# Optimization experiments

Measured on AMD Instinct MI355X. Metric: run time of the kernel, lower is better.

The kernel has to match this reference:

```python
import jax, jax.numpy as jnp
import numpy as np

B, H, N = 128, 512, 1024

def setup_inputs() -> dict:
    key = jax.random.key(0)
    ks = jax.random.split(key, 9)
    s = 1.0 / np.sqrt(H)
    return {
        "mc_hidden": jax.random.normal(ks[0], (B, H), jnp.float32),
        "sn_hidden": jax.random.normal(ks[1], (B, H, N), jnp.float32),
        "attn_W": jax.random.normal(ks[2], (H, 2 * H), jnp.float32) * s,
        "attn_v": jax.random.normal(ks[3], (H,), jnp.float32) * s,
        "ptr_v": jax.random.normal(ks[4], (H,), jnp.float32) * s,
        "fc1_W": jax.random.normal(ks[5], (H, 2 * H), jnp.float32) * s,
        "fc1_b": jax.random.normal(ks[6], (H,), jnp.float32) * s,
        "fc2_W": jax.random.normal(ks[7], (H, H), jnp.float32) * s,
        "fc2_b": jax.random.normal(ks[8], (H,), jnp.float32) * s,
    }


def reference(mc_hidden, sn_hidden, attn_W, attn_v, ptr_v, fc1_W, fc1_b, fc2_W, fc2_b):
    # ---- Attention (Bahdanau-style additive scoring) ----
    # hidden: (B, 2H, N) = cat(sn_hidden, mc expanded along N) on dim 1
    mc_exp = jnp.broadcast_to(mc_hidden[:, :, None], sn_hidden.shape)  # (B,H,N)
    hidden = jnp.concatenate((sn_hidden, mc_exp), axis=1)              # (B,2H,N)
    # W @ hidden -> (B,H,N); v @ tanh(.) -> (B,N)
    scores = jnp.einsum('h,bhn->bn', attn_v,
                        jnp.tanh(jnp.einsum('hk,bkn->bhn', attn_W, hidden)))
    attns = jax.nn.softmax(scores, axis=-1)                            # (B,N)
    # ---- Context + pointer scoring ----
    context = jnp.einsum('bn,bhn->bh', attns, sn_hidden)               # (B,H)
    x = jnp.concatenate((mc_hidden, context), axis=1)                  # (B,2H)
    out = jax.nn.relu(x @ fc1_W.T + fc1_b)                             # (B,H)
    out = jax.nn.relu(out @ fc2_W.T + fc2_b)                           # (B,H)
    probs = jnp.einsum('h,bhn->bn', ptr_v,
                       jnp.tanh(sn_hidden + out[:, :, None]))          # (B,N)
    return probs
```

## Files before the change

### kernel.cpp

```cpp
#include <hip/hip_runtime.h>
#include <hip/hip_bf16.h>

#define Bn 128
#define Hd 512
#define Nn 1024

typedef __attribute__((ext_vector_type(8))) short short8;
typedef __attribute__((ext_vector_type(4))) float f32x4;

#define GLOAD_LDS16(gptr, lptr)                                                     \
    __builtin_amdgcn_global_load_lds(                                               \
        (const __attribute__((address_space(1))) void*)(gptr),                      \
        (__attribute__((address_space(3))) void*)(lptr), 16, 0, 0)

__device__ __forceinline__ unsigned pack_bf2(float a, float b) {
    __hip_bfloat162 h = __float22bfloat162_rn(float2{a, b});
    unsigned u;
    __builtin_memcpy(&u, &h, 4);
    return u;
}

__device__ __forceinline__ float wave_sum(float v) {
    v += __shfl_xor(v, 32);
    v += __shfl_xor(v, 16);
    v += __shfl_xor(v, 8);
    v += __shfl_xor(v, 4);
    v += __shfl_xor(v, 2);
    v += __shfl_xor(v, 1);
    return v;
}

__device__ __forceinline__ float tanh_fast(float x) {
    float e = __expf(2.0f * x);
    return 1.0f - 2.0f * __builtin_amdgcn_rcpf(e + 1.0f);
}

__global__ void pre_kernel(const float* __restrict__ attn_W,
                           const float* __restrict__ mc,
                           unsigned short* __restrict__ Wb,
                           float* __restrict__ mc_term) {
    if (blockIdx.x < 128) {
        int idx = (blockIdx.x * 256 + threadIdx.x) * 8;
        int h = idx >> 9;
        int k = idx & 511;
        const float* p = attn_W + (size_t)h * 1024 + k;
        float4 v0 = *(const float4*)p;
        float4 v1 = *(const float4*)(p + 4);
        unsigned u[4] = {pack_bf2(v0.x, v0.y), pack_bf2(v0.z, v0.w),
                         pack_bf2(v1.x, v1.y), pack_bf2(v1.z, v1.w)};
        *(uint4*)(Wb + idx) = *(uint4*)u;
        return;
    }
    int wg = ((blockIdx.x - 128) * 256 + threadIdx.x) >> 6;
    int lane = threadIdx.x & 63;
    int b = wg >> 9;
    int h = wg & 511;
    const float* m = mc + b * Hd + lane * 8;
    const float* w = attn_W + (size_t)h * 1024 + 512 + lane * 8;
    float4 m0 = *(const float4*)m, m1 = *(const float4*)(m + 4);
    float4 w0 = *(const float4*)w, w1 = *(const float4*)(w + 4);
    float acc = m0.x * w0.x + m0.y * w0.y + m0.z * w0.z + m0.w * w0.w +
                m1.x * w1.x + m1.y * w1.y + m1.z * w1.z + m1.w * w1.w;
    acc = wave_sum(acc);
    if (lane == 0) mc_term[b * Hd + h] = acc;
}

__global__ __launch_bounds__(512, 4)
void attn_score_kernel(const float* __restrict__ sn,
                       const unsigned short* __restrict__ Wb,
                       const float* __restrict__ attn_v,
                       const float* __restrict__ mc_term,
                       float* __restrict__ scores_part) {
    __shared__ __align__(16) unsigned short A_lds[256 * 64];
    __shared__ __align__(16) unsigned short B_lds[128 * 64];
    __shared__ float av_s[256];
    __shared__ float mct_s[256];
    __shared__ float ssum[128];

    const int bid = blockIdx.x;
    const int b = bid >> 4;
    const int mh = (bid >> 3) & 1;
    const int n0 = (bid & 7) << 7;
    const int tid = threadIdx.x;
    const int lane = tid & 63;
    const int wid = tid >> 6;
    const int wr = wid >> 1;
    const int wc = wid & 1;
    const int quad = lane >> 4;
    const int l15 = lane & 15;

    if (tid < 256) {
        av_s[tid] = attn_v[mh * 256 + tid];
        mct_s[tid] = mc_term[b * Hd + mh * 256 + tid];
    }
    if (tid < 128) ssum[tid] = 0.f;

    f32x4 acc[4][4];
#pragma unroll
    for (int i = 0; i < 4; ++i)
#pragma unroll
        for (int j = 0; j < 4; ++j) {
            f32x4 z = {0.f, 0.f, 0.f, 0.f};
            acc[i][j] = z;
        }

    const int r8 = lane >> 3;
    const int csw = ((lane & 7) ^ r8) * 16;
    const char* Wg = (const char*)Wb + (size_t)(mh * 256) * 1024;
    const int key = l15 & 7;

    const int bswz = ((wid ^ (lane & 7)) * 16);
    const float* snB = sn + (size_t)b * Hd * Nn + (size_t)(8 * wid) * Nn + n0 + lane;

    for (int k0 = 0; k0 < 512; k0 += 64) {
#pragma unroll
        for (int i = 0; i < 4; ++i) {
            const int row = wid * 32 + i * 8;
            GLOAD_LDS16(Wg + (size_t)(row + r8) * 1024 + k0 * 2 + csw,
                        (char*)A_lds + row * 128);
        }
        {
            const float* pk = snB + (size_t)k0 * Nn;
#pragma unroll
            for (int j = 0; j < 2; ++j) {
                const int n = lane + 64 * j;
                const float* p = pk + 64 * j;
                float v0 = p[0 * Nn], v1 = p[1 * Nn], v2 = p[2 * Nn], v3 = p[3 * Nn];
                float v4 = p[4 * Nn], v5 = p[5 * Nn], v6 = p[6 * Nn], v7 = p[7 * Nn];
                unsigned kp[4] = {pack_bf2(v0, v1), pack_bf2(v2, v3),
                                  pack_bf2(v4, v5), pack_bf2(v6, v7)};
                *(uint4*)((char*)B_lds + n * 128 + bswz) = *(uint4*)kp;
            }
        }
        __syncthreads();
        __builtin_amdgcn_s_setprio(1);
#pragma unroll
        for (int kk = 0; kk < 2; ++kk) {
            const int cb = quad + kk * 4;
            short8 bfr[4], afr[4];
#pragma unroll
            for (int nt = 0; nt < 4; ++nt) {
                const int nl = wc * 64 + nt * 16 + l15;
                bfr[nt] = *(const short8*)((const char*)B_lds + nl * 128 + ((cb ^ key) * 16));
            }
#pragma unroll
            for (int mt = 0; mt < 4; ++mt) {
                const int m = wr * 64 + mt * 16 + l15;
                afr[mt] = *(const short8*)((const char*)A_lds + m * 128 + ((cb ^ key) * 16));
            }
#pragma unroll
            for (int mt = 0; mt < 4; ++mt)
#pragma unroll
                for (int nt = 0; nt < 4; ++nt)
                    acc[mt][nt] = __builtin_amdgcn_mfma_f32_16x16x32_bf16(afr[mt], bfr[nt], acc[mt][nt], 0, 0, 0);
        }
        __builtin_amdgcn_s_setprio(0);
        __syncthreads();
    }

    float s[4] = {0.f, 0.f, 0.f, 0.f};
#pragma unroll
    for (int mt = 0; mt < 4; ++mt) {
        int hb = wr * 64 + mt * 16 + quad * 4;
#pragma unroll
        for (int r = 0; r < 4; ++r) {
            float av = av_s[hb + r];
            float mcv = mct_s[hb + r];
#pragma unroll
            for (int nt = 0; nt < 4; ++nt)
                s[nt] += av * tanh_fast(acc[mt][nt][r] + mcv);
        }
    }
#pragma unroll
    for (int nt = 0; nt < 4; ++nt) {
        float v = s[nt];
        v += __shfl_xor(v, 16);
        v += __shfl_xor(v, 32);
        if (lane < 16) atomicAdd(&ssum[wc * 64 + nt * 16 + l15], v);
    }
    __syncthreads();
    if (tid < 128)
        scores_part[((size_t)mh * Bn + b) * Nn + n0 + tid] = ssum[tid];
}

__global__ void softmax_context_kernel(const float* __restrict__ sn,
                                       const float* __restrict__ scores_part,
                                       float* __restrict__ context) {
    int b = blockIdx.x >> 3;
    int h0 = (blockIdx.x & 7) << 6;
    int t = threadIdx.x;
    int lane = t & 63, wid = t >> 6;
    __shared__ float red[4];
    __shared__ float a_s[1024];

    const float* s0 = scores_part + (size_t)b * Nn;
    const float* s1 = scores_part + ((size_t)Bn + b) * Nn;
    float v[4];
#pragma unroll
    for (int i = 0; i < 4; ++i) {
        int idx = t + i * 256;
        v[i] = s0[idx] + s1[idx];
    }
    float m = fmaxf(fmaxf(v[0], v[1]), fmaxf(v[2], v[3]));
#pragma unroll
    for (int off = 32; off >= 1; off >>= 1) m = fmaxf(m, __shfl_xor(m, off));
    if (lane == 0) red[wid] = m;
    __syncthreads();
    m = fmaxf(fmaxf(red[0], red[1]), fmaxf(red[2], red[3]));
    __syncthreads();
    float s = 0.f;
#pragma unroll
    for (int i = 0; i < 4; ++i) {
        v[i] = __expf(v[i] - m);
        s += v[i];
    }
    s = wave_sum(s);
    if (lane == 0) red[wid] = s;
    __syncthreads();
    s = red[0] + red[1] + red[2] + red[3];
    float inv = __builtin_amdgcn_rcpf(s);
#pragma unroll
    for (int i = 0; i < 4; ++i) a_s[t + i * 256] = v[i] * inv;
    __syncthreads();

    int h = h0 + (t >> 2), q = t & 3;
    const float* row = sn + ((size_t)b * Hd + h) * Nn;
    float acc = 0.f;
#pragma unroll 8
    for (int j = 0; j < 64; ++j) {
        int n = q * 4 + j * 16;
        float4 f = *(const float4*)&row[n];
        float4 a = *(const float4*)&a_s[n];
        acc += f.x * a.x + f.y * a.y + f.z * a.z + f.w * a.w;
    }
    acc += __shfl_xor(acc, 1);
    acc += __shfl_xor(acc, 2);
    if (q == 0) context[b * Hd + h] = acc;
}

__global__ void fc1_kernel(const float* __restrict__ mc,
                           const float* __restrict__ ctx,
                           const float* __restrict__ fc1_W,
                           const float* __restrict__ fc1_b,
                           float* __restrict__ out1) {
    int wg = (blockIdx.x * blockDim.x + threadIdx.x) >> 6;
    int lane = threadIdx.x & 63;
    int b = wg >> 9, h = wg & 511;
    const float* wr = fc1_W + (size_t)h * 1024;
    float acc = 0.f;
    {
        float4 w0 = *(const float4*)(wr + lane * 8);
        float4 w1 = *(const float4*)(wr + lane * 8 + 4);
        float4 x0 = *(const float4*)(mc + b * Hd + lane * 8);
        float4 x1 = *(const float4*)(mc + b * Hd + lane * 8 + 4);
        acc += w0.x * x0.x + w0.y * x0.y + w0.z * x0.z + w0.w * x0.w;
        acc += w1.x * x1.x + w1.y * x1.y + w1.z * x1.z + w1.w * x1.w;
    }
    {
        float4 w0 = *(const float4*)(wr + 512 + lane * 8);
        float4 w1 = *(const float4*)(wr + 512 + lane * 8 + 4);
        float4 x0 = *(const float4*)(ctx + b * Hd + lane * 8);
        float4 x1 = *(const float4*)(ctx + b * Hd + lane * 8 + 4);
        acc += w0.x * x0.x + w0.y * x0.y + w0.z * x0.z + w0.w * x0.w;
        acc += w1.x * x1.x + w1.y * x1.y + w1.z * x1.z + w1.w * x1.w;
    }
    acc = wave_sum(acc);
    if (lane == 0) out1[b * Hd + h] = fmaxf(acc + fc1_b[h], 0.f);
}

__global__ void fc2_kernel(const float* __restrict__ out1,
                           const float* __restrict__ fc2_W,
                           const float* __restrict__ fc2_b,
                           float* __restrict__ out2) {
    int wg = (blockIdx.x * blockDim.x + threadIdx.x) >> 6;
    int lane = threadIdx.x & 63;
    int b = wg >> 9, h = wg & 511;
    const float* wr = fc2_W + (size_t)h * 512 + lane * 8;
    float4 w0 = *(const float4*)wr;
    float4 w1 = *(const float4*)(wr + 4);
    float4 x0 = *(const float4*)(out1 + b * Hd + lane * 8);
    float4 x1 = *(const float4*)(out1 + b * Hd + lane * 8 + 4);
    float acc = w0.x * x0.x + w0.y * x0.y + w0.z * x0.z + w0.w * x0.w +
                w1.x * x1.x + w1.y * x1.y + w1.z * x1.z + w1.w * x1.w;
    acc = wave_sum(acc);
    if (lane == 0) out2[b * Hd + h] = fmaxf(acc + fc2_b[h], 0.f);
}

__global__ void final_kernel(const float* __restrict__ sn,
                             const float* __restrict__ ptr_v,
                             const float* __restrict__ out2,
                             float* __restrict__ probs) {
    int b = blockIdx.x >> 2;
    int n0 = (blockIdx.x & 3) << 8;
    int t = threadIdx.x;
    int w = t >> 6, l = t & 63;
    __shared__ float pv_s[512], o2_s[512];
    __shared__ float fsum[4][256];
    pv_s[t] = ptr_v[t];
    pv_s[t + 256] = ptr_v[t + 256];
    o2_s[t] = out2[b * Hd + t];
    o2_s[t + 256] = out2[b * Hd + t + 256];
    __syncthreads();
    const float* col = sn + (size_t)b * Hd * Nn + n0 + l * 4;
    float a0 = 0.f, a1 = 0.f, a2 = 0.f, a3 = 0.f;
#pragma unroll 4
    for (int j = 0; j < 128; ++j) {
        int h = w * 128 + j;
        float4 f = *(const float4*)&col[(size_t)h * Nn];
        float p = pv_s[h], o = o2_s[h];
        a0 += p * tanh_fast(f.x + o);
        a1 += p * tanh_fast(f.y + o);
        a2 += p * tanh_fast(f.z + o);
        a3 += p * tanh_fast(f.w + o);
    }
    fsum[w][l * 4 + 0] = a0;
    fsum[w][l * 4 + 1] = a1;
    fsum[w][l * 4 + 2] = a2;
    fsum[w][l * 4 + 3] = a3;
    __syncthreads();
    float r = fsum[0][t & 255] + fsum[1][t & 255] + fsum[2][t & 255] + fsum[3][t & 255];
    probs[b * Nn + n0 + (t & 255)] = r;
}

extern "C" void kernel_launch(void* const* d_in, const int* in_sizes, int n_in,
                              void* d_out, int out_size, void* d_ws, size_t ws_size,
                              hipStream_t stream) {
    const float* mc  = (const float*)d_in[0];
    const float* sn  = (const float*)d_in[1];
    const float* aW  = (const float*)d_in[2];
    const float* av  = (const float*)d_in[3];
    const float* pv  = (const float*)d_in[4];
    const float* f1W = (const float*)d_in[5];
    const float* f1b = (const float*)d_in[6];
    const float* f2W = (const float*)d_in[7];
    const float* f2b = (const float*)d_in[8];

    unsigned short* Wb = (unsigned short*)d_ws;
    float* fws         = (float*)(Wb + 512 * 512);
    float* mc_term     = fws;
    float* scores_part = mc_term + Bn * Hd;
    float* context     = scores_part + 2 * Bn * Nn;
    float* out1        = context + Bn * Hd;
    float* out2        = out1 + Bn * Hd;
    float* probs       = (float*)d_out;

    pre_kernel<<<dim3(16512), dim3(256), 0, stream>>>(aW, mc, Wb, mc_term);
    attn_score_kernel<<<dim3(2048), dim3(512), 0, stream>>>(sn, Wb, av, mc_term, scores_part);
    softmax_context_kernel<<<dim3(1024), dim3(256), 0, stream>>>(sn, scores_part, context);
    fc1_kernel<<<dim3(16384), dim3(256), 0, stream>>>(mc, context, f1W, f1b, out1);
    fc2_kernel<<<dim3(16384), dim3(256), 0, stream>>>(out1, f2W, f2b, out2);
    final_kernel<<<dim3(512), dim3(256), 0, stream>>>(sn, pv, out2, probs);
}
```

Before: 535.9 us.

## Pre-transpose sn to bf16 N-major and load GEMM B tiles via direct LDS loads

Adds a separate kernel that converts sn to bf16 and transposes it to a [b][n][k] layout in workspace. The attention-score GEMM can then fetch B tiles with async global-to-LDS loads instead of strided fp32 reads followed by register packing. The score kernel is reshaped to 256 threads with 64-column tiles, and block IDs are remapped so that blocks sharing a batch stay on the same XCD. The cost is an extra full pass that reads 256MB of sn and writes 128MB of bf16, and the s_setprio hints are removed.

```diff
diff --git a/kernel.cpp b/kernel.cpp
--- a/kernel.cpp
+++ b/kernel.cpp
@@ -65,35 +65,74 @@
     if (lane == 0) mc_term[b * Hd + h] = acc;
 }
 
-__global__ __launch_bounds__(512, 4)
-void attn_score_kernel(const float* __restrict__ sn,
+__global__ void transpose_sn_kernel(const float* __restrict__ sn,
+                                    unsigned short* __restrict__ snT) {
+    __shared__ unsigned ldsb[32 * 132];
+    int bid = blockIdx.x;
+    int b = bid >> 6;
+    int kt = (bid >> 3) & 7;
+    int nt = bid & 7;
+    int k0 = kt << 6, n0 = nt << 7;
+    int t = threadIdx.x;
+
+    int kp_l = t >> 5;
+    int n4 = (t & 31) * 4;
+#pragma unroll
+    for (int j = 0; j < 4; ++j) {
+        int kp = j * 8 + kp_l;
+        const float* p0 = sn + ((size_t)(b * Hd + k0 + 2 * kp)) * Nn + n0 + n4;
+        float4 f0 = *(const float4*)p0;
+        float4 f1 = *(const float4*)(p0 + Nn);
+        unsigned u[4];
+        u[0] = pack_bf2(f0.x, f1.x);
+        u[1] = pack_bf2(f0.y, f1.y);
+        u[2] = pack_bf2(f0.z, f1.z);
+        u[3] = pack_bf2(f0.w, f1.w);
+        *(uint4*)&ldsb[kp * 132 + n4] = *(uint4*)u;
+    }
+    __syncthreads();
+
+    int c = t & 7;
+#pragma unroll
+    for (int it = 0; it < 4; ++it) {
+        int n = (t >> 3) + it * 32;
+        unsigned u[4];
+#pragma unroll
+        for (int i = 0; i < 4; ++i) u[i] = ldsb[(c * 4 + i) * 132 + n];
+        unsigned short* dst = snT + ((size_t)(b * Nn) + n0 + n) * Hd + k0 + c * 8;
+        *(uint4*)dst = *(uint4*)u;
+    }
+}
+
+__global__ __launch_bounds__(256, 3)
+void attn_score_kernel(const unsigned short* __restrict__ snT,
                        const unsigned short* __restrict__ Wb,
                        const float* __restrict__ attn_v,
                        const float* __restrict__ mc_term,
                        float* __restrict__ scores_part) {
     __shared__ __align__(16) unsigned short A_lds[256 * 64];
-    __shared__ __align__(16) unsigned short B_lds[128 * 64];
+    __shared__ __align__(16) unsigned short B_lds[64 * 64];
     __shared__ float av_s[256];
     __shared__ float mct_s[256];
-    __shared__ float ssum[128];
+    __shared__ float ssum[64];
 
     const int bid = blockIdx.x;
-    const int b = bid >> 4;
-    const int mh = (bid >> 3) & 1;
-    const int n0 = (bid & 7) << 7;
+    const int xcd = bid & 7;
+    const int ixd = bid >> 3;
+    const int mh = ixd & 1;
+    const int pair = xcd * 256 + (ixd >> 1);
+    const int b = pair >> 4;
+    const int n0 = (pair & 15) << 6;
+
     const int tid = threadIdx.x;
     const int lane = tid & 63;
     const int wid = tid >> 6;
-    const int wr = wid >> 1;
-    const int wc = wid & 1;
     const int quad = lane >> 4;
     const int l15 = lane & 15;
 
-    if (tid < 256) {
-        av_s[tid] = attn_v[mh * 256 + tid];
-        mct_s[tid] = mc_term[b * Hd + mh * 256 + tid];
-    }
-    if (tid < 128) ssum[tid] = 0.f;
+    av_s[tid] = attn_v[mh * 256 + tid];
+    mct_s[tid] = mc_term[b * Hd + mh * 256 + tid];
+    if (tid < 64) ssum[tid] = 0.f;
 
     f32x4 acc[4][4];
 #pragma unroll
@@ -107,45 +146,35 @@
     const int r8 = lane >> 3;
     const int csw = ((lane & 7) ^ r8) * 16;
     const char* Wg = (const char*)Wb + (size_t)(mh * 256) * 1024;
+    const char* Bg = (const char*)snT + ((size_t)(b * Nn + n0)) * 1024;
     const int key = l15 & 7;
 
-    const int bswz = ((wid ^ (lane & 7)) * 16);
-    const float* snB = sn + (size_t)b * Hd * Nn + (size_t)(8 * wid) * Nn + n0 + lane;
-
     for (int k0 = 0; k0 < 512; k0 += 64) {
 #pragma unroll
-        for (int i = 0; i < 4; ++i) {
-            const int row = wid * 32 + i * 8;
+        for (int i = 0; i < 8; ++i) {
+            const int row = wid * 64 + i * 8;
             GLOAD_LDS16(Wg + (size_t)(row + r8) * 1024 + k0 * 2 + csw,
                         (char*)A_lds + row * 128);
         }
-        {
-            const float* pk = snB + (size_t)k0 * Nn;
-#pragma unroll
-            for (int j = 0; j < 2; ++j) {
-                const int n = lane + 64 * j;
-                const float* p = pk + 64 * j;
-                float v0 = p[0 * Nn], v1 = p[1 * Nn], v2 = p[2 * Nn], v3 = p[3 * Nn];
-                float v4 = p[4 * Nn], v5 = p[5 * Nn], v6 = p[6 * Nn], v7 = p[7 * Nn];
-                unsigned kp[4] = {pack_bf2(v0, v1), pack_bf2(v2, v3),
-                                  pack_bf2(v4, v5), pack_bf2(v6, v7)};
-                *(uint4*)((char*)B_lds + n * 128 + bswz) = *(uint4*)kp;
-            }
+#pragma unroll
+        for (int i = 0; i < 2; ++i) {
+            const int row = wid * 16 + i * 8;
+            GLOAD_LDS16(Bg + (size_t)(row + r8) * 1024 + k0 * 2 + csw,
+                        (char*)B_lds + row * 128);
         }
         __syncthreads();
-        __builtin_amdgcn_s_setprio(1);
 #pragma unroll
         for (int kk = 0; kk < 2; ++kk) {
             const int cb = quad + kk * 4;
             short8 bfr[4], afr[4];
 #pragma unroll
             for (int nt = 0; nt < 4; ++nt) {
-                const int nl = wc * 64 + nt * 16 + l15;
-                bfr[nt] = *(const short8*)((const char*)B_lds + nl * 128 + ((cb ^ key) * 16));
+                const int n = nt * 16 + l15;
+                bfr[nt] = *(const short8*)((const char*)B_lds + n * 128 + ((cb ^ key) * 16));
             }
 #pragma unroll
             for (int mt = 0; mt < 4; ++mt) {
-                const int m = wr * 64 + mt * 16 + l15;
+                const int m = wid * 64 + mt * 16 + l15;
                 afr[mt] = *(const short8*)((const char*)A_lds + m * 128 + ((cb ^ key) * 16));
             }
 #pragma unroll
@@ -154,14 +183,13 @@
                 for (int nt = 0; nt < 4; ++nt)
                     acc[mt][nt] = __builtin_amdgcn_mfma_f32_16x16x32_bf16(afr[mt], bfr[nt], acc[mt][nt], 0, 0, 0);
         }
-        __builtin_amdgcn_s_setprio(0);
         __syncthreads();
     }
 
     float s[4] = {0.f, 0.f, 0.f, 0.f};
 #pragma unroll
     for (int mt = 0; mt < 4; ++mt) {
-        int hb = wr * 64 + mt * 16 + quad * 4;
+        int hb = wid * 64 + mt * 16 + quad * 4;
 #pragma unroll
         for (int r = 0; r < 4; ++r) {
             float av = av_s[hb + r];
@@ -176,10 +204,10 @@
         float v = s[nt];
         v += __shfl_xor(v, 16);
         v += __shfl_xor(v, 32);
-        if (lane < 16) atomicAdd(&ssum[wc * 64 + nt * 16 + l15], v);
-    }
-    __syncthreads();
-    if (tid < 128)
+        if (lane < 16) atomicAdd(&ssum[nt * 16 + l15], v);
+    }
+    __syncthreads();
+    if (tid < 64)
         scores_part[((size_t)mh * Bn + b) * Nn + n0 + tid] = ssum[tid];
 }
 
@@ -335,17 +363,19 @@
     const float* f2W = (const float*)d_in[7];
     const float* f2b = (const float*)d_in[8];
 
-    unsigned short* Wb = (unsigned short*)d_ws;
-    float* fws         = (float*)(Wb + 512 * 512);
-    float* mc_term     = fws;
-    float* scores_part = mc_term + Bn * Hd;
-    float* context     = scores_part + 2 * Bn * Nn;
-    float* out1        = context + Bn * Hd;
-    float* out2        = out1 + Bn * Hd;
-    float* probs       = (float*)d_out;
-
+    unsigned short* snT = (unsigned short*)d_ws;
+    unsigned short* Wb  = snT + (size_t)Bn * Nn * Hd;
+    float* fws          = (float*)(Wb + 512 * 512);
+    float* mc_term      = fws;
+    float* scores_part  = mc_term + Bn * Hd;
+    float* context      = scores_part + 2 * Bn * Nn;
+    float* out1         = context + Bn * Hd;
+    float* out2         = out1 + Bn * Hd;
+    float* probs        = (float*)d_out;
+
+    transpose_sn_kernel<<<dim3(8192), dim3(256), 0, stream>>>(sn, snT);
     pre_kernel<<<dim3(16512), dim3(256), 0, stream>>>(aW, mc, Wb, mc_term);
-    attn_score_kernel<<<dim3(2048), dim3(512), 0, stream>>>(sn, Wb, av, mc_term, scores_part);
+    attn_score_kernel<<<dim3(4096), dim3(256), 0, stream>>>(snT, Wb, av, mc_term, scores_part);
     softmax_context_kernel<<<dim3(1024), dim3(256), 0, stream>>>(sn, scores_part, context);
     fc1_kernel<<<dim3(16384), dim3(256), 0, stream>>>(mc, context, f1W, f1b, out1);
     fc2_kernel<<<dim3(16384), dim3(256), 0, stream>>>(out1, f2W, f2b, out2);
```

Measured after the change: 618.5 us. 1.15x slower.

## Split attention score GEMM into 128-row H tiles with 256-thread blocks

Applied to the files above, without the earlier changes.

The attention score kernel now splits H into four 128-row tiles instead of two 256-row tiles and runs 256 threads per block, so it launches twice as many smaller blocks. Block indices are reordered so the n-tile is the slowest dimension. The B-tile load is remapped to the new thread count, four partial score buffers are summed in the softmax kernel, and the setprio hints are dropped. The smaller tiles are meant to raise occupancy and scheduling flexibility. In exchange, each sn tile is read and converted to bf16 twice as often, and there are more partial-score writes.

```diff
diff --git a/kernel.cpp b/kernel.cpp
--- a/kernel.cpp
+++ b/kernel.cpp
@@ -65,22 +65,25 @@
     if (lane == 0) mc_term[b * Hd + h] = acc;
 }
 
-__global__ __launch_bounds__(512, 4)
+__global__ __launch_bounds__(256, 3)
 void attn_score_kernel(const float* __restrict__ sn,
                        const unsigned short* __restrict__ Wb,
                        const float* __restrict__ attn_v,
                        const float* __restrict__ mc_term,
                        float* __restrict__ scores_part) {
-    __shared__ __align__(16) unsigned short A_lds[256 * 64];
+    __shared__ __align__(16) unsigned short A_lds[128 * 64];
     __shared__ __align__(16) unsigned short B_lds[128 * 64];
-    __shared__ float av_s[256];
-    __shared__ float mct_s[256];
+    __shared__ float av_s[128];
+    __shared__ float mct_s[128];
     __shared__ float ssum[128];
 
     const int bid = blockIdx.x;
-    const int b = bid >> 4;
-    const int mh = (bid >> 3) & 1;
-    const int n0 = (bid & 7) << 7;
+    const int nt = bid >> 9;
+    const int rb = bid & 511;
+    const int b = rb >> 2;
+    const int mh = rb & 3;
+    const int n0 = nt << 7;
+
     const int tid = threadIdx.x;
     const int lane = tid & 63;
     const int wid = tid >> 6;
@@ -89,11 +92,11 @@
     const int quad = lane >> 4;
     const int l15 = lane & 15;
 
-    if (tid < 256) {
-        av_s[tid] = attn_v[mh * 256 + tid];
-        mct_s[tid] = mc_term[b * Hd + mh * 256 + tid];
-    }
-    if (tid < 128) ssum[tid] = 0.f;
+    if (tid < 128) {
+        av_s[tid] = attn_v[mh * 128 + tid];
+        mct_s[tid] = mc_term[b * Hd + mh * 128 + tid];
+        ssum[tid] = 0.f;
+    }
 
     f32x4 acc[4][4];
 #pragma unroll
@@ -106,11 +109,13 @@
 
     const int r8 = lane >> 3;
     const int csw = ((lane & 7) ^ r8) * 16;
-    const char* Wg = (const char*)Wb + (size_t)(mh * 256) * 1024;
+    const char* Wg = (const char*)Wb + (size_t)(mh * 128) * 1024;
     const int key = l15 & 7;
 
-    const int bswz = ((wid ^ (lane & 7)) * 16);
-    const float* snB = sn + (size_t)b * Hd * Nn + (size_t)(8 * wid) * Nn + n0 + lane;
+    const int cB = tid >> 5;
+    const int nbB = tid & 31;
+    const int bswz = ((cB ^ (nbB & 7)) * 16);
+    const float* snB = sn + (size_t)b * Hd * Nn + n0 + nbB + (size_t)(8 * cB) * Nn;
 
     for (int k0 = 0; k0 < 512; k0 += 64) {
 #pragma unroll
@@ -122,9 +127,9 @@
         {
             const float* pk = snB + (size_t)k0 * Nn;
 #pragma unroll
-            for (int j = 0; j < 2; ++j) {
-                const int n = lane + 64 * j;
-                const float* p = pk + 64 * j;
+            for (int j = 0; j < 4; ++j) {
+                const int n = nbB + 32 * j;
+                const float* p = pk + 32 * j;
                 float v0 = p[0 * Nn], v1 = p[1 * Nn], v2 = p[2 * Nn], v3 = p[3 * Nn];
                 float v4 = p[4 * Nn], v5 = p[5 * Nn], v6 = p[6 * Nn], v7 = p[7 * Nn];
                 unsigned kp[4] = {pack_bf2(v0, v1), pack_bf2(v2, v3),
@@ -133,15 +138,14 @@
             }
         }
         __syncthreads();
-        __builtin_amdgcn_s_setprio(1);
 #pragma unroll
         for (int kk = 0; kk < 2; ++kk) {
             const int cb = quad + kk * 4;
             short8 bfr[4], afr[4];
 #pragma unroll
-            for (int nt = 0; nt < 4; ++nt) {
-                const int nl = wc * 64 + nt * 16 + l15;
-                bfr[nt] = *(const short8*)((const char*)B_lds + nl * 128 + ((cb ^ key) * 16));
+            for (int ntt = 0; ntt < 4; ++ntt) {
+                const int nl = wc * 64 + ntt * 16 + l15;
+                bfr[ntt] = *(const short8*)((const char*)B_lds + nl * 128 + ((cb ^ key) * 16));
             }
 #pragma unroll
             for (int mt = 0; mt < 4; ++mt) {
@@ -151,10 +155,9 @@
 #pragma unroll
             for (int mt = 0; mt < 4; ++mt)
 #pragma unroll
-                for (int nt = 0; nt < 4; ++nt)
-                    acc[mt][nt] = __builtin_amdgcn_mfma_f32_16x16x32_bf16(afr[mt], bfr[nt], acc[mt][nt], 0, 0, 0);
-        }
-        __builtin_amdgcn_s_setprio(0);
+                for (int ntt = 0; ntt < 4; ++ntt)
+                    acc[mt][ntt] = __builtin_amdgcn_mfma_f32_16x16x32_bf16(afr[mt], bfr[ntt], acc[mt][ntt], 0, 0, 0);
+        }
         __syncthreads();
     }
 
@@ -167,16 +170,16 @@
             float av = av_s[hb + r];
             float mcv = mct_s[hb + r];
 #pragma unroll
-            for (int nt = 0; nt < 4; ++nt)
-                s[nt] += av * tanh_fast(acc[mt][nt][r] + mcv);
-        }
-    }
-#pragma unroll
-    for (int nt = 0; nt < 4; ++nt) {
-        float v = s[nt];
+            for (int ntt = 0; ntt < 4; ++ntt)
+                s[ntt] += av * tanh_fast(acc[mt][ntt][r] + mcv);
+        }
+    }
+#pragma unroll
+    for (int ntt = 0; ntt < 4; ++ntt) {
+        float v = s[ntt];
         v += __shfl_xor(v, 16);
         v += __shfl_xor(v, 32);
-        if (lane < 16) atomicAdd(&ssum[wc * 64 + nt * 16 + l15], v);
+        if (lane < 16) atomicAdd(&ssum[wc * 64 + ntt * 16 + l15], v);
     }
     __syncthreads();
     if (tid < 128)
@@ -195,11 +198,13 @@
 
     const float* s0 = scores_part + (size_t)b * Nn;
     const float* s1 = scores_part + ((size_t)Bn + b) * Nn;
+    const float* s2 = scores_part + ((size_t)2 * Bn + b) * Nn;
+    const float* s3 = scores_part + ((size_t)3 * Bn + b) * Nn;
     float v[4];
 #pragma unroll
     for (int i = 0; i < 4; ++i) {
         int idx = t + i * 256;
-        v[i] = s0[idx] + s1[idx];
+        v[i] = (s0[idx] + s1[idx]) + (s2[idx] + s3[idx]);
     }
     float m = fmaxf(fmaxf(v[0], v[1]), fmaxf(v[2], v[3]));
 #pragma unroll
@@ -339,13 +344,13 @@
     float* fws         = (float*)(Wb + 512 * 512);
     float* mc_term     = fws;
     float* scores_part = mc_term + Bn * Hd;
-    float* context     = scores_part + 2 * Bn * Nn;
+    float* context     = scores_part + 4 * Bn * Nn;
     float* out1        = context + Bn * Hd;
     float* out2        = out1 + Bn * Hd;
     float* probs       = (float*)d_out;
 
     pre_kernel<<<dim3(16512), dim3(256), 0, stream>>>(aW, mc, Wb, mc_term);
-    attn_score_kernel<<<dim3(2048), dim3(512), 0, stream>>>(sn, Wb, av, mc_term, scores_part);
+    attn_score_kernel<<<dim3(4096), dim3(256), 0, stream>>>(sn, Wb, av, mc_term, scores_part);
     softmax_context_kernel<<<dim3(1024), dim3(256), 0, stream>>>(sn, scores_part, context);
     fc1_kernel<<<dim3(16384), dim3(256), 0, stream>>>(mc, context, f1W, f1b, out1);
     fc2_kernel<<<dim3(16384), dim3(256), 0, stream>>>(out1, f2W, f2b, out2);
```

After: 588.5 us. 9.8% more time.
